# Performance work log

Measured on AMD Instinct MI355X. Metric: run time of the kernel, lower is better.

Reference implementation:

```python
import jax, jax.numpy as jnp
import numpy as np

B, D, L, H = 2, 64, 512, 1024  # batch, n_docs (timesteps), tokens per doc, bert hidden


def _ln(x, g, b):
    # torch.nn.LayerNorm over last dim, eps=1e-5
    m = jnp.mean(x, axis=-1, keepdims=True)
    v = jnp.mean((x - m) ** 2, axis=-1, keepdims=True)
    return (x - m) / jnp.sqrt(v + 1e-5) * g + b


def _ht(x):
    # Hardtanh(min=-8, max=8)
    return jnp.clip(x, -8.0, 8.0)


def setup_inputs() -> dict:
    key = jax.random.key(0)
    ks = jax.random.split(key, 12)
    xavier = lambda k, shape: jax.random.normal(k, shape, dtype=jnp.float32) * np.float32(np.sqrt(2.0 / sum(shape)))
    return {
        "trans": jax.random.normal(ks[0], (B, D, L, H), dtype=jnp.float32) * 0.1,  # frozen BERT last_hidden_state
        "document_mask": jax.random.bernoulli(ks[1], 0.9, (B, D)),
        "Wf": xavier(ks[2], (H, H)), "bf": jnp.ones((H,), jnp.float32),
        "Wi": xavier(ks[3], (H, H)), "bi": jnp.zeros((H,), jnp.float32),
        "Wg": xavier(ks[4], (H, H)), "bg": jnp.zeros((H,), jnp.float32),
        "Wo": xavier(ks[5], (H, H)), "bo": jnp.zeros((H,), jnp.float32),
        "Wp": xavier(ks[6], (H, H)), "bp": jnp.zeros((H,), jnp.float32),
        "tF": xavier(ks[7], (L,)), "tI": xavier(ks[8], (L,)), "tO": xavier(ks[9], (L,)),
        "c_gamma": jnp.ones((H,), jnp.float32), "c_beta": jnp.zeros((H,), jnp.float32),
        "h_gamma": jnp.ones((H,), jnp.float32), "h_beta": jnp.zeros((H,), jnp.float32),
    }


def _forward(trans, document_mask, Wf, bf, Wi, bi, Wg, bg, Wo, bo, Wp, bp,
             tF, tI, tO, c_gamma, c_beta, h_gamma, h_beta):
    b, d, l, h = trans.shape
    # docFlat @ transform: contract the token (l) axis -> [b, d, h]
    pF = jnp.einsum('bdlh,l->bdh', trans, tF)
    pI = jnp.einsum('bdlh,l->bdh', trans, tI)
    pO = jnp.einsum('bdlh,l->bdh', trans, tO)

    def step(carry, xs):
        c, hs = carry                      # each [b, h]
        pf, pi, po, m = xs                 # [b, h] x3, [b] bool
        nC = _ln(c, c_gamma, c_beta)
        nH = _ln(hs, h_gamma, h_beta)
        f = jax.nn.sigmoid(_ht(nH @ Wf.T + bf) + pf)
        c2 = c * f
        i = jax.nn.sigmoid(_ht(nH @ Wi.T + bi) + pi)
        g = _ht(jax.nn.gelu(nH @ Wg.T + bg, approximate=False) + pi)
        c2 = c2 + i * g
        o = jax.nn.sigmoid(_ht(nH @ Wo.T + bo) + po)
        h2 = o * _ht(jax.nn.gelu(nC @ Wp.T + bp, approximate=False))
        mm = m[:, None]
        h2 = jnp.where(mm, h2, hs)
        c2 = jnp.where(mm, c2, c)
        c2 = jnp.clip(c2, -10.0, 10.0)
        h2 = jnp.clip(h2, -10.0, 10.0)
        return (c2, h2), None

    init = (jnp.zeros((b, h), trans.dtype), jnp.zeros((b, h), trans.dtype))
    xs = (pF.transpose(1, 0, 2), pI.transpose(1, 0, 2), pO.transpose(1, 0, 2), document_mask.T)
    (c_fin, h_fin), _ = jax.lax.scan(step, init, xs)
    return h_fin  # [b, h] (original returns [b, h, 1])


def reference(trans, document_mask, Wf, bf, Wi, bi, Wg, bg, Wo, bo, Wp, bp,
              tF, tI, tO, c_gamma, c_beta, h_gamma, h_beta):
    return _forward(trans, document_mask, Wf, bf, Wi, bi, Wg, bg, Wo, bo, Wp, bp,
                    tF, tI, tO, c_gamma, c_beta, h_gamma, h_beta)
```

## Files before the change

### kernel.cpp

```cpp
#include <hip/hip_runtime.h>
#include <math.h>


#define NBLK 256
typedef unsigned long long u64;

__device__ __forceinline__ float sigf(float x)   { return 1.0f / (1.0f + __expf(-x)); }
__device__ __forceinline__ float geluf(float x)  { return 0.5f * x * (1.0f + erff(x * 0.70710678118654752f)); }
__device__ __forceinline__ float clampf(float x, float lo, float hi) { return fminf(fmaxf(x, lo), hi); }

__device__ __forceinline__ void astf(float* p, float v) {
    __hip_atomic_store(p, v, __ATOMIC_RELAXED, __HIP_MEMORY_SCOPE_AGENT);
}
__device__ __forceinline__ float aldf(const float* p) {
    return __hip_atomic_load(p, __ATOMIC_RELAXED, __HIP_MEMORY_SCOPE_AGENT);
}
__device__ __forceinline__ void astu(unsigned* p, unsigned v) {
    __hip_atomic_store(p, v, __ATOMIC_RELAXED, __HIP_MEMORY_SCOPE_AGENT);
}
__device__ __forceinline__ unsigned aldu(const unsigned* p) {
    return __hip_atomic_load(p, __ATOMIC_RELAXED, __HIP_MEMORY_SCOPE_AGENT);
}
__device__ __forceinline__ void ast64(u64* p, u64 v) {
    __hip_atomic_store(p, v, __ATOMIC_RELAXED, __HIP_MEMORY_SCOPE_AGENT);
}
__device__ __forceinline__ u64 ald64(const u64* p) {
    return __hip_atomic_load(p, __ATOMIC_RELAXED, __HIP_MEMORY_SCOPE_AGENT);
}

__device__ __forceinline__ void gridbar(unsigned tgt, unsigned* flags, unsigned* rel,
                                        int blk, int t) {
    __syncthreads();
    if (t == 0) astu(&flags[blk], tgt);
    if (blk == 0) {
        if (t < 64) {
            for (;;) {
                unsigned a = aldu(&flags[t]);
                unsigned b = aldu(&flags[t + 64]);
                unsigned c = aldu(&flags[t + 128]);
                unsigned d = aldu(&flags[t + 192]);
                int ok = (a >= tgt) && (b >= tgt) && (c >= tgt) && (d >= tgt);
                if (__all(ok)) break;
                __builtin_amdgcn_s_sleep(1);
            }
            if (t == 0) astu(rel, tgt);
        }
    } else if (t == 0) {
        while (aldu(rel) < tgt) __builtin_amdgcn_s_sleep(2);
    }
    __syncthreads();
}

__global__ __launch_bounds__(256, 1) void fused_kernel(
    const float* __restrict__ trans, const int* __restrict__ mask,
    const float* __restrict__ Wf, const float* __restrict__ bf,
    const float* __restrict__ Wi, const float* __restrict__ bi,
    const float* __restrict__ Wg, const float* __restrict__ bg,
    const float* __restrict__ Wo, const float* __restrict__ bo,
    const float* __restrict__ Wp, const float* __restrict__ bp,
    const float* __restrict__ tF, const float* __restrict__ tI, const float* __restrict__ tO,
    const float* __restrict__ c_gamma, const float* __restrict__ c_beta,
    const float* __restrict__ h_gamma, const float* __restrict__ h_beta,
    float* __restrict__ ws, float* __restrict__ out)
{
    const int t    = threadIdx.x;
    const int lane = t & 63;
    const int wv   = t >> 6;
    const int blk  = blockIdx.x;
    const int hrow = (blk << 2) + wv;

    unsigned* flags = (unsigned*)ws;
    unsigned* rel   = flags + 256;
    u64* stC2 = (u64*)(ws + 320);
    u64* stH2 = (u64*)(ws + 8512);
    float* pF  = ws + 16704;
    float* pI  = pF + 131072;
    float* pO  = pI + 131072;

    __shared__ float smem[2][4][1024];
    __shared__ float red[2][4][8];

    float4 wfr[4], wir[4], wgr[4], wor[4], wpr[4];
    {
        const float4* rf = (const float4*)(Wf + (size_t)hrow * 1024);
        const float4* ri = (const float4*)(Wi + (size_t)hrow * 1024);
        const float4* rg = (const float4*)(Wg + (size_t)hrow * 1024);
        const float4* ro = (const float4*)(Wo + (size_t)hrow * 1024);
        const float4* rp = (const float4*)(Wp + (size_t)hrow * 1024);
        #pragma unroll
        for (int q = 0; q < 4; ++q) {
            const int k4 = lane + 64 * q;
            wfr[q] = rf[k4]; wir[q] = ri[k4]; wgr[q] = rg[k4];
            wor[q] = ro[k4]; wpr[q] = rp[k4];
        }
    }
    const float bfv = bf[hrow], biv = bi[hrow], bgv = bg[hrow], bov = bo[hrow], bpv = bp[hrow];

    {
        float* sF = &smem[0][0][0];
        float* sI = &smem[0][0][512];
        float* sO = &smem[0][1][0];
        sF[t] = tF[t]; sF[t + 256] = tF[t + 256];
        sI[t] = tI[t]; sI[t + 256] = tI[t + 256];
        sO[t] = tO[t]; sO[t + 256] = tO[t + 256];
        __syncthreads();

        const int bd = blk >> 1;
        const int h0 = (blk & 1) * 512;
        const int s  = t & 127;
        const int g  = t >> 7;
        const float4* tr = (const float4*)trans + (size_t)bd * 512 * 256 + (h0 >> 2) + s;

        float4 aF = make_float4(0.f,0.f,0.f,0.f);
        float4 aI = make_float4(0.f,0.f,0.f,0.f);
        float4 aO = make_float4(0.f,0.f,0.f,0.f);
        #pragma unroll 8
        for (int li = 0; li < 256; ++li) {
            const int l = g + 2 * li;
            float4 v = tr[(size_t)l * 256];
            const float wf = sF[l], wi = sI[l], wo = sO[l];
            aF.x = fmaf(v.x, wf, aF.x); aF.y = fmaf(v.y, wf, aF.y);
            aF.z = fmaf(v.z, wf, aF.z); aF.w = fmaf(v.w, wf, aF.w);
            aI.x = fmaf(v.x, wi, aI.x); aI.y = fmaf(v.y, wi, aI.y);
            aI.z = fmaf(v.z, wi, aI.z); aI.w = fmaf(v.w, wi, aI.w);
            aO.x = fmaf(v.x, wo, aO.x); aO.y = fmaf(v.y, wo, aO.y);
            aO.z = fmaf(v.z, wo, aO.z); aO.w = fmaf(v.w, wo, aO.w);
        }
        float4* cmb = (float4*)&smem[0][2][0];
        if (g == 1) { cmb[s] = aF; cmb[128 + s] = aI; cmb[256 + s] = aO; }
        __syncthreads();
        if (g == 0) {
            const float4 bF = cmb[s], bI = cmb[128 + s], bO = cmb[256 + s];
            aF.x += bF.x; aF.y += bF.y; aF.z += bF.z; aF.w += bF.w;
            aI.x += bI.x; aI.y += bI.y; aI.z += bI.z; aI.w += bI.w;
            aO.x += bO.x; aO.y += bO.y; aO.z += bO.z; aO.w += bO.w;
            const int base = bd * 1024 + h0 + 4 * s;
            astf(&pF[base+0], aF.x); astf(&pF[base+1], aF.y);
            astf(&pF[base+2], aF.z); astf(&pF[base+3], aF.w);
            astf(&pI[base+0], aI.x); astf(&pI[base+1], aI.y);
            astf(&pI[base+2], aI.z); astf(&pI[base+3], aI.w);
            astf(&pO[base+0], aO.x); astf(&pO[base+1], aO.y);
            astf(&pO[base+2], aO.z); astf(&pO[base+3], aO.w);
        }
    }
    gridbar(1u, flags, rel, blk, t);

    float cgv[4], cbv[4], hgv[4], hbv[4];
    #pragma unroll
    for (int j = 0; j < 4; ++j) {
        const int e = t + 256 * j;
        cgv[j] = c_gamma[e]; cbv[j] = c_beta[e];
        hgv[j] = h_gamma[e]; hbv[j] = h_beta[e];
    }

    for (int d = 0; d < 64; ++d) {
        const int par = d & 1;
        const u64* cc2 = stC2 + par * 2048;
        const u64* hc2 = stH2 + par * 2048;
        u64* cn2 = stC2 + (par ^ 1) * 2048;
        u64* hn2 = stH2 + (par ^ 1) * 2048;
        float (*sm)[1024] = smem[par];
        float (*rd)[8]    = red[par];

        float pfv = 0.f, piv = 0.f, pov = 0.f;
        if (lane < 2) {
            const int pidx = (lane * 64 + d) * 1024 + hrow;
            pfv = aldf(&pF[pidx]); piv = aldf(&pI[pidx]); pov = aldf(&pO[pidx]);
        }

        u64 vc0[4], vc1[4], vh0[4], vh1[4];
        u64 vco = 0, vho = 0;
        const unsigned dtag = (unsigned)d;
        for (;;) {
            #pragma unroll
            for (int j = 0; j < 4; ++j) {
                const int e = t + 256 * j;
                vc0[j] = ald64(cc2 + e);        vc1[j] = ald64(cc2 + 1024 + e);
                vh0[j] = ald64(hc2 + e);        vh1[j] = ald64(hc2 + 1024 + e);
            }
            bool ok = true;
            #pragma unroll
            for (int j = 0; j < 4; ++j) {
                ok = ok && ((unsigned)(vc0[j] >> 32) == dtag) && ((unsigned)(vc1[j] >> 32) == dtag)
                        && ((unsigned)(vh0[j] >> 32) == dtag) && ((unsigned)(vh1[j] >> 32) == dtag);
            }
            if (lane < 2) {
                vco = ald64(cc2 + lane * 1024 + hrow);
                vho = ald64(hc2 + lane * 1024 + hrow);
                ok = ok && ((unsigned)(vco >> 32) == dtag) && ((unsigned)(vho >> 32) == dtag);
            }
            if (ok) break;
            __builtin_amdgcn_s_sleep(1);
        }

        float cv0[4], cv1[4], hv0[4], hv1[4];
        float s0=0,s1=0,s2=0,s3=0,s4=0,s5=0,s6=0,s7=0;
        #pragma unroll
        for (int j = 0; j < 4; ++j) {
            cv0[j] = __uint_as_float((unsigned)vc0[j]);
            cv1[j] = __uint_as_float((unsigned)vc1[j]);
            hv0[j] = __uint_as_float((unsigned)vh0[j]);
            hv1[j] = __uint_as_float((unsigned)vh1[j]);
            s0 += cv0[j]; s1 += cv0[j]*cv0[j];
            s2 += cv1[j]; s3 += cv1[j]*cv1[j];
            s4 += hv0[j]; s5 += hv0[j]*hv0[j];
            s6 += hv1[j]; s7 += hv1[j]*hv1[j];
        }
        #pragma unroll
        for (int off = 32; off; off >>= 1) {
            s0 += __shfl_xor(s0, off); s1 += __shfl_xor(s1, off);
            s2 += __shfl_xor(s2, off); s3 += __shfl_xor(s3, off);
            s4 += __shfl_xor(s4, off); s5 += __shfl_xor(s5, off);
            s6 += __shfl_xor(s6, off); s7 += __shfl_xor(s7, off);
        }
        if (lane == 0) {
            rd[wv][0]=s0; rd[wv][1]=s1; rd[wv][2]=s2; rd[wv][3]=s3;
            rd[wv][4]=s4; rd[wv][5]=s5; rd[wv][6]=s6; rd[wv][7]=s7;
        }
        __syncthreads();
        const float tc0 = rd[0][0]+rd[1][0]+rd[2][0]+rd[3][0];
        const float qc0 = rd[0][1]+rd[1][1]+rd[2][1]+rd[3][1];
        const float tc1 = rd[0][2]+rd[1][2]+rd[2][2]+rd[3][2];
        const float qc1 = rd[0][3]+rd[1][3]+rd[2][3]+rd[3][3];
        const float th0 = rd[0][4]+rd[1][4]+rd[2][4]+rd[3][4];
        const float qh0 = rd[0][5]+rd[1][5]+rd[2][5]+rd[3][5];
        const float th1 = rd[0][6]+rd[1][6]+rd[2][6]+rd[3][6];
        const float qh1 = rd[0][7]+rd[1][7]+rd[2][7]+rd[3][7];
        const float inv = 1.0f / 1024.0f;
        const float mc0 = tc0*inv, rc0 = rsqrtf(qc0*inv - mc0*mc0 + 1e-5f);
        const float mc1 = tc1*inv, rc1 = rsqrtf(qc1*inv - mc1*mc1 + 1e-5f);
        const float mh0 = th0*inv, rh0 = rsqrtf(qh0*inv - mh0*mh0 + 1e-5f);
        const float mh1 = th1*inv, rh1 = rsqrtf(qh1*inv - mh1*mh1 + 1e-5f);

        #pragma unroll
        for (int j = 0; j < 4; ++j) {
            const int e = t + 256 * j;
            sm[0][e] = (hv0[j]-mh0)*rh0*hgv[j] + hbv[j];
            sm[1][e] = (hv1[j]-mh1)*rh1*hgv[j] + hbv[j];
            sm[2][e] = (cv0[j]-mc0)*rc0*cgv[j] + cbv[j];
            sm[3][e] = (cv1[j]-mc1)*rc1*cgv[j] + cbv[j];
        }
        __syncthreads();

        float zf0=0,zf1=0,zi0=0,zi1=0,zg0=0,zg1=0,zo0=0,zo1=0,zp0=0,zp1=0;
        #pragma unroll
        for (int q = 0; q < 4; ++q) {
            const int k4 = lane + 64 * q;
            const float4 n0 = ((const float4*)sm[0])[k4];
            const float4 n1 = ((const float4*)sm[1])[k4];
            const float4 m0 = ((const float4*)sm[2])[k4];
            const float4 m1 = ((const float4*)sm[3])[k4];
            zf0 += wfr[q].x*n0.x + wfr[q].y*n0.y + wfr[q].z*n0.z + wfr[q].w*n0.w;
            zf1 += wfr[q].x*n1.x + wfr[q].y*n1.y + wfr[q].z*n1.z + wfr[q].w*n1.w;
            zi0 += wir[q].x*n0.x + wir[q].y*n0.y + wir[q].z*n0.z + wir[q].w*n0.w;
            zi1 += wir[q].x*n1.x + wir[q].y*n1.y + wir[q].z*n1.z + wir[q].w*n1.w;
            zg0 += wgr[q].x*n0.x + wgr[q].y*n0.y + wgr[q].z*n0.z + wgr[q].w*n0.w;
            zg1 += wgr[q].x*n1.x + wgr[q].y*n1.y + wgr[q].z*n1.z + wgr[q].w*n1.w;
            zo0 += wor[q].x*n0.x + wor[q].y*n0.y + wor[q].z*n0.z + wor[q].w*n0.w;
            zo1 += wor[q].x*n1.x + wor[q].y*n1.y + wor[q].z*n1.z + wor[q].w*n1.w;
            zp0 += wpr[q].x*m0.x + wpr[q].y*m0.y + wpr[q].z*m0.z + wpr[q].w*m0.w;
            zp1 += wpr[q].x*m1.x + wpr[q].y*m1.y + wpr[q].z*m1.z + wpr[q].w*m1.w;
        }
        #pragma unroll
        for (int off = 32; off; off >>= 1) {
            zf0 += __shfl_xor(zf0, off); zf1 += __shfl_xor(zf1, off);
            zi0 += __shfl_xor(zi0, off); zi1 += __shfl_xor(zi1, off);
            zg0 += __shfl_xor(zg0, off); zg1 += __shfl_xor(zg1, off);
            zo0 += __shfl_xor(zo0, off); zo1 += __shfl_xor(zo1, off);
            zp0 += __shfl_xor(zp0, off); zp1 += __shfl_xor(zp1, off);
        }

        if (lane < 2) {
            const int b = lane;
            const float zf = b ? zf1 : zf0;
            const float zi = b ? zi1 : zi0;
            const float zg = b ? zg1 : zg0;
            const float zo = b ? zo1 : zo0;
            const float zp = b ? zp1 : zp0;
            const float f  = sigf(clampf(zf + bfv, -8.f, 8.f) + pfv);
            const float ig = sigf(clampf(zi + biv, -8.f, 8.f) + piv);
            const float g  = clampf(geluf(zg + bgv) + piv, -8.f, 8.f);
            const float o  = sigf(clampf(zo + bov, -8.f, 8.f) + pov);
            const float hp = clampf(geluf(zp + bpv), -8.f, 8.f);
            const float co = __uint_as_float((unsigned)vco);
            const float ho = __uint_as_float((unsigned)vho);
            float c2 = co * f + ig * g;
            float h2 = o * hp;
            if (mask[b * 64 + d] == 0) { c2 = co; h2 = ho; }
            c2 = clampf(c2, -10.f, 10.f);
            h2 = clampf(h2, -10.f, 10.f);
            if (d == 63) {
                out[b * 1024 + hrow] = h2;
            } else {
                const u64 tg = ((u64)(unsigned)(d + 1)) << 32;
                ast64(cn2 + b * 1024 + hrow, tg | (u64)__float_as_uint(c2));
                ast64(hn2 + b * 1024 + hrow, tg | (u64)__float_as_uint(h2));
            }
        }
    }
}

extern "C" void kernel_launch(void* const* d_in, const int* in_sizes, int n_in,
                              void* d_out, int out_size, void* d_ws, size_t ws_size,
                              hipStream_t stream)
{
    const float* trans = (const float*)d_in[0];
    const int*   mask  = (const int*)d_in[1];
    const float* Wf = (const float*)d_in[2];  const float* bf = (const float*)d_in[3];
    const float* Wi = (const float*)d_in[4];  const float* bi = (const float*)d_in[5];
    const float* Wg = (const float*)d_in[6];  const float* bg = (const float*)d_in[7];
    const float* Wo = (const float*)d_in[8];  const float* bo = (const float*)d_in[9];
    const float* Wp = (const float*)d_in[10]; const float* bp = (const float*)d_in[11];
    const float* tF = (const float*)d_in[12];
    const float* tI = (const float*)d_in[13];
    const float* tO = (const float*)d_in[14];
    const float* c_gamma = (const float*)d_in[15];
    const float* c_beta  = (const float*)d_in[16];
    const float* h_gamma = (const float*)d_in[17];
    const float* h_beta  = (const float*)d_in[18];

    float* ws  = (float*)d_ws;
    float* out = (float*)d_out;

    hipMemsetAsync(d_ws, 0, 16704u * sizeof(float), stream);

    void* args[] = { (void*)&trans, (void*)&mask,
                     (void*)&Wf, (void*)&bf, (void*)&Wi, (void*)&bi,
                     (void*)&Wg, (void*)&bg, (void*)&Wo, (void*)&bo,
                     (void*)&Wp, (void*)&bp,
                     (void*)&tF, (void*)&tI, (void*)&tO,
                     (void*)&c_gamma, (void*)&c_beta, (void*)&h_gamma, (void*)&h_beta,
                     (void*)&ws, (void*)&out };
    hipLaunchCooperativeKernel((void*)fused_kernel, dim3(256), dim3(256), args, 0, stream);
}
```

Before: 966.5 us.

## Replace tagged 64-bit state polling with per-block flag barrier and fold LayerNorm into weights

Each step now waits on a per-block flag array polled by one wave, instead of every thread spinning on tag-packed 64-bit state loads. Plain 32-bit state values are read after the flag check. LayerNorm gamma/beta are folded into the register-resident weight rows once, and mean/rstd are applied to the dot-product results as a scalar correction. This drops a shared-memory pass and a __syncthreads per step. Per-step synchronization now needs a full flag wait plus extra block barriers, and the algebraic LayerNorm fold can change rounding slightly.

```diff
diff --git a/kernel.cpp b/kernel.cpp
--- a/kernel.cpp
+++ b/kernel.cpp
@@ -3,7 +3,6 @@
 
 
 #define NBLK 256
-typedef unsigned long long u64;
 
 __device__ __forceinline__ float sigf(float x)   { return 1.0f / (1.0f + __expf(-x)); }
 __device__ __forceinline__ float geluf(float x)  { return 0.5f * x * (1.0f + erff(x * 0.70710678118654752f)); }
@@ -20,35 +19,6 @@
 }
 __device__ __forceinline__ unsigned aldu(const unsigned* p) {
     return __hip_atomic_load(p, __ATOMIC_RELAXED, __HIP_MEMORY_SCOPE_AGENT);
-}
-__device__ __forceinline__ void ast64(u64* p, u64 v) {
-    __hip_atomic_store(p, v, __ATOMIC_RELAXED, __HIP_MEMORY_SCOPE_AGENT);
-}
-__device__ __forceinline__ u64 ald64(const u64* p) {
-    return __hip_atomic_load(p, __ATOMIC_RELAXED, __HIP_MEMORY_SCOPE_AGENT);
-}
-
-__device__ __forceinline__ void gridbar(unsigned tgt, unsigned* flags, unsigned* rel,
-                                        int blk, int t) {
-    __syncthreads();
-    if (t == 0) astu(&flags[blk], tgt);
-    if (blk == 0) {
-        if (t < 64) {
-            for (;;) {
-                unsigned a = aldu(&flags[t]);
-                unsigned b = aldu(&flags[t + 64]);
-                unsigned c = aldu(&flags[t + 128]);
-                unsigned d = aldu(&flags[t + 192]);
-                int ok = (a >= tgt) && (b >= tgt) && (c >= tgt) && (d >= tgt);
-                if (__all(ok)) break;
-                __builtin_amdgcn_s_sleep(1);
-            }
-            if (t == 0) astu(rel, tgt);
-        }
-    } else if (t == 0) {
-        while (aldu(rel) < tgt) __builtin_amdgcn_s_sleep(2);
-    }
-    __syncthreads();
 }
 
 __global__ __launch_bounds__(256, 1) void fused_kernel(
@@ -70,10 +40,9 @@
     const int hrow = (blk << 2) + wv;
 
     unsigned* flags = (unsigned*)ws;
-    unsigned* rel   = flags + 256;
-    u64* stC2 = (u64*)(ws + 320);
-    u64* stH2 = (u64*)(ws + 8512);
-    float* pF  = ws + 16704;
+    float* stC = ws + 320;
+    float* stH = ws + 4416;
+    float* pF  = ws + 8512;
     float* pI  = pF + 131072;
     float* pO  = pI + 131072;
 
@@ -143,64 +112,117 @@
             astf(&pO[base+2], aO.z); astf(&pO[base+3], aO.w);
         }
     }
-    gridbar(1u, flags, rel, blk, t);
-
-    float cgv[4], cbv[4], hgv[4], hbv[4];
-    #pragma unroll
-    for (int j = 0; j < 4; ++j) {
-        const int e = t + 256 * j;
-        cgv[j] = c_gamma[e]; cbv[j] = c_beta[e];
-        hgv[j] = h_gamma[e]; hbv[j] = h_beta[e];
-    }
+    __syncthreads();
+    if (t == 0) astu(&flags[blk], 1u);
+
+    float sfv, siv, sgv, sov, spv, bfb, bib, bgb, bob, bpb;
+    {
+        float4 gh4[4], bh4[4], gc4[4], bc4[4];
+        const float4* Gh = (const float4*)h_gamma;
+        const float4* Bh = (const float4*)h_beta;
+        const float4* Gc = (const float4*)c_gamma;
+        const float4* Bc = (const float4*)c_beta;
+        #pragma unroll
+        for (int q = 0; q < 4; ++q) {
+            const int k4 = lane + 64 * q;
+            gh4[q] = Gh[k4]; bh4[q] = Bh[k4]; gc4[q] = Gc[k4]; bc4[q] = Bc[k4];
+        }
+        bfb = bib = bgb = bob = bpb = 0.f;
+        #pragma unroll
+        for (int q = 0; q < 4; ++q) {
+            bfb += wfr[q].x*bh4[q].x + wfr[q].y*bh4[q].y + wfr[q].z*bh4[q].z + wfr[q].w*bh4[q].w;
+            bib += wir[q].x*bh4[q].x + wir[q].y*bh4[q].y + wir[q].z*bh4[q].z + wir[q].w*bh4[q].w;
+            bgb += wgr[q].x*bh4[q].x + wgr[q].y*bh4[q].y + wgr[q].z*bh4[q].z + wgr[q].w*bh4[q].w;
+            bob += wor[q].x*bh4[q].x + wor[q].y*bh4[q].y + wor[q].z*bh4[q].z + wor[q].w*bh4[q].w;
+            bpb += wpr[q].x*bc4[q].x + wpr[q].y*bc4[q].y + wpr[q].z*bc4[q].z + wpr[q].w*bc4[q].w;
+        }
+        #pragma unroll
+        for (int q = 0; q < 4; ++q) {
+            wfr[q].x *= gh4[q].x; wfr[q].y *= gh4[q].y; wfr[q].z *= gh4[q].z; wfr[q].w *= gh4[q].w;
+            wir[q].x *= gh4[q].x; wir[q].y *= gh4[q].y; wir[q].z *= gh4[q].z; wir[q].w *= gh4[q].w;
+            wgr[q].x *= gh4[q].x; wgr[q].y *= gh4[q].y; wgr[q].z *= gh4[q].z; wgr[q].w *= gh4[q].w;
+            wor[q].x *= gh4[q].x; wor[q].y *= gh4[q].y; wor[q].z *= gh4[q].z; wor[q].w *= gh4[q].w;
+            wpr[q].x *= gc4[q].x; wpr[q].y *= gc4[q].y; wpr[q].z *= gc4[q].z; wpr[q].w *= gc4[q].w;
+        }
+        sfv = siv = sgv = sov = spv = 0.f;
+        #pragma unroll
+        for (int q = 0; q < 4; ++q) {
+            sfv += wfr[q].x + wfr[q].y + wfr[q].z + wfr[q].w;
+            siv += wir[q].x + wir[q].y + wir[q].z + wir[q].w;
+            sgv += wgr[q].x + wgr[q].y + wgr[q].z + wgr[q].w;
+            sov += wor[q].x + wor[q].y + wor[q].z + wor[q].w;
+            spv += wpr[q].x + wpr[q].y + wpr[q].z + wpr[q].w;
+        }
+        #pragma unroll
+        for (int off = 32; off; off >>= 1) {
+            sfv += __shfl_xor(sfv, off); siv += __shfl_xor(siv, off);
+            sgv += __shfl_xor(sgv, off); sov += __shfl_xor(sov, off);
+            spv += __shfl_xor(spv, off);
+            bfb += __shfl_xor(bfb, off); bib += __shfl_xor(bib, off);
+            bgb += __shfl_xor(bgb, off); bob += __shfl_xor(bob, off);
+            bpb += __shfl_xor(bpb, off);
+        }
+    }
+
+    if (wv == 0) {
+        for (;;) {
+            const unsigned a0 = aldu(&flags[lane]);
+            const unsigned a1 = aldu(&flags[lane + 64]);
+            const unsigned a2 = aldu(&flags[lane + 128]);
+            const unsigned a3 = aldu(&flags[lane + 192]);
+            const int ok = (a0 >= 1u) && (a1 >= 1u) && (a2 >= 1u) && (a3 >= 1u);
+            if (__all(ok)) break;
+            __builtin_amdgcn_s_sleep(1);
+        }
+    }
+    __syncthreads();
+
+    float c_prev = 0.f, h_prev = 0.f;
 
     for (int d = 0; d < 64; ++d) {
         const int par = d & 1;
-        const u64* cc2 = stC2 + par * 2048;
-        const u64* hc2 = stH2 + par * 2048;
-        u64* cn2 = stC2 + (par ^ 1) * 2048;
-        u64* hn2 = stH2 + (par ^ 1) * 2048;
+        const float* cc = stC + par * 2048;
+        const float* hc = stH + par * 2048;
+        float* cn = stC + (par ^ 1) * 2048;
+        float* hn = stH + (par ^ 1) * 2048;
         float (*sm)[1024] = smem[par];
         float (*rd)[8]    = red[par];
 
         float pfv = 0.f, piv = 0.f, pov = 0.f;
+        int mv = 1;
         if (lane < 2) {
             const int pidx = (lane * 64 + d) * 1024 + hrow;
             pfv = aldf(&pF[pidx]); piv = aldf(&pI[pidx]); pov = aldf(&pO[pidx]);
-        }
-
-        u64 vc0[4], vc1[4], vh0[4], vh1[4];
-        u64 vco = 0, vho = 0;
-        const unsigned dtag = (unsigned)d;
-        for (;;) {
-            #pragma unroll
-            for (int j = 0; j < 4; ++j) {
-                const int e = t + 256 * j;
-                vc0[j] = ald64(cc2 + e);        vc1[j] = ald64(cc2 + 1024 + e);
-                vh0[j] = ald64(hc2 + e);        vh1[j] = ald64(hc2 + 1024 + e);
+            mv = mask[lane * 64 + d];
+        }
+
+        if (wv == 0) {
+            const unsigned tgt = (unsigned)(d + 1);
+            for (;;) {
+                const unsigned a0 = aldu(&flags[lane]);
+                const unsigned a1 = aldu(&flags[lane + 64]);
+                const unsigned a2 = aldu(&flags[lane + 128]);
+                const unsigned a3 = aldu(&flags[lane + 192]);
+                const int ok = (a0 >= tgt) && (a1 >= tgt) && (a2 >= tgt) && (a3 >= tgt);
+                if (__all(ok)) break;
+                __builtin_amdgcn_s_sleep(1);
             }
-            bool ok = true;
-            #pragma unroll
-            for (int j = 0; j < 4; ++j) {
-                ok = ok && ((unsigned)(vc0[j] >> 32) == dtag) && ((unsigned)(vc1[j] >> 32) == dtag)
-                        && ((unsigned)(vh0[j] >> 32) == dtag) && ((unsigned)(vh1[j] >> 32) == dtag);
-            }
-            if (lane < 2) {
-                vco = ald64(cc2 + lane * 1024 + hrow);
-                vho = ald64(hc2 + lane * 1024 + hrow);
-                ok = ok && ((unsigned)(vco >> 32) == dtag) && ((unsigned)(vho >> 32) == dtag);
-            }
-            if (ok) break;
-            __builtin_amdgcn_s_sleep(1);
-        }
+        }
+        __syncthreads();
 
         float cv0[4], cv1[4], hv0[4], hv1[4];
+        #pragma unroll
+        for (int j = 0; j < 4; ++j) {
+            const int e = t + 256 * j;
+            cv0[j] = aldf(cc + e);        cv1[j] = aldf(cc + 1024 + e);
+            hv0[j] = aldf(hc + e);        hv1[j] = aldf(hc + 1024 + e);
+        }
         float s0=0,s1=0,s2=0,s3=0,s4=0,s5=0,s6=0,s7=0;
         #pragma unroll
         for (int j = 0; j < 4; ++j) {
-            cv0[j] = __uint_as_float((unsigned)vc0[j]);
-            cv1[j] = __uint_as_float((unsigned)vc1[j]);
-            hv0[j] = __uint_as_float((unsigned)vh0[j]);
-            hv1[j] = __uint_as_float((unsigned)vh1[j]);
+            const int e = t + 256 * j;
+            sm[0][e] = hv0[j]; sm[1][e] = hv1[j];
+            sm[2][e] = cv0[j]; sm[3][e] = cv1[j];
             s0 += cv0[j]; s1 += cv0[j]*cv0[j];
             s2 += cv1[j]; s3 += cv1[j]*cv1[j];
             s4 += hv0[j]; s5 += hv0[j]*hv0[j];
@@ -218,6 +240,7 @@
             rd[wv][4]=s4; rd[wv][5]=s5; rd[wv][6]=s6; rd[wv][7]=s7;
         }
         __syncthreads();
+
         const float tc0 = rd[0][0]+rd[1][0]+rd[2][0]+rd[3][0];
         const float qc0 = rd[0][1]+rd[1][1]+rd[2][1]+rd[3][1];
         const float tc1 = rd[0][2]+rd[1][2]+rd[2][2]+rd[3][2];
@@ -231,16 +254,6 @@
         const float mc1 = tc1*inv, rc1 = rsqrtf(qc1*inv - mc1*mc1 + 1e-5f);
         const float mh0 = th0*inv, rh0 = rsqrtf(qh0*inv - mh0*mh0 + 1e-5f);
         const float mh1 = th1*inv, rh1 = rsqrtf(qh1*inv - mh1*mh1 + 1e-5f);
-
-        #pragma unroll
-        for (int j = 0; j < 4; ++j) {
-            const int e = t + 256 * j;
-            sm[0][e] = (hv0[j]-mh0)*rh0*hgv[j] + hbv[j];
-            sm[1][e] = (hv1[j]-mh1)*rh1*hgv[j] + hbv[j];
-            sm[2][e] = (cv0[j]-mc0)*rc0*cgv[j] + cbv[j];
-            sm[3][e] = (cv1[j]-mc1)*rc1*cgv[j] + cbv[j];
-        }
-        __syncthreads();
 
         float zf0=0,zf1=0,zi0=0,zi1=0,zg0=0,zg1=0,zo0=0,zo1=0,zp0=0,zp1=0;
         #pragma unroll
@@ -272,31 +285,35 @@
 
         if (lane < 2) {
             const int b = lane;
-            const float zf = b ? zf1 : zf0;
-            const float zi = b ? zi1 : zi0;
-            const float zg = b ? zg1 : zg0;
-            const float zo = b ? zo1 : zo0;
-            const float zp = b ? zp1 : zp0;
+            const float mh = b ? mh1 : mh0, rh = b ? rh1 : rh0;
+            const float mc = b ? mc1 : mc0, rc = b ? rc1 : rc0;
+            const float zf = rh * ((b ? zf1 : zf0) - mh * sfv) + bfb;
+            const float zi = rh * ((b ? zi1 : zi0) - mh * siv) + bib;
+            const float zg = rh * ((b ? zg1 : zg0) - mh * sgv) + bgb;
+            const float zo = rh * ((b ? zo1 : zo0) - mh * sov) + bob;
+            const float zp = rc * ((b ? zp1 : zp0) - mc * spv) + bpb;
             const float f  = sigf(clampf(zf + bfv, -8.f, 8.f) + pfv);
             const float ig = sigf(clampf(zi + biv, -8.f, 8.f) + piv);
             const float g  = clampf(geluf(zg + bgv) + piv, -8.f, 8.f);
             const float o  = sigf(clampf(zo + bov, -8.f, 8.f) + pov);
             const float hp = clampf(geluf(zp + bpv), -8.f, 8.f);
-            const float co = __uint_as_float((unsigned)vco);
-            const float ho = __uint_as_float((unsigned)vho);
-            float c2 = co * f + ig * g;
+            float c2 = c_prev * f + ig * g;
             float h2 = o * hp;
-            if (mask[b * 64 + d] == 0) { c2 = co; h2 = ho; }
+            if (mv == 0) { c2 = c_prev; h2 = h_prev; }
             c2 = clampf(c2, -10.f, 10.f);
             h2 = clampf(h2, -10.f, 10.f);
+            c_prev = c2; h_prev = h2;
             if (d == 63) {
                 out[b * 1024 + hrow] = h2;
             } else {
-                const u64 tg = ((u64)(unsigned)(d + 1)) << 32;
-                ast64(cn2 + b * 1024 + hrow, tg | (u64)__float_as_uint(c2));
-                ast64(hn2 + b * 1024 + hrow, tg | (u64)__float_as_uint(h2));
+                astf(cn + b * 1024 + hrow, c2);
+                astf(hn + b * 1024 + hrow, h2);
             }
         }
+
+        if (d == 63) break;
+        __syncthreads();
+        if (t == 0) astu(&flags[blk], (unsigned)(d + 2));
     }
 }
 
@@ -322,7 +339,7 @@
     float* ws  = (float*)d_ws;
     float* out = (float*)d_out;
 
-    hipMemsetAsync(d_ws, 0, 16704u * sizeof(float), stream);
+    hipMemsetAsync(d_ws, 0, 8512u * sizeof(float), stream);
 
     void* args[] = { (void*)&trans, (void*)&mask,
                      (void*)&Wf, (void*)&bf, (void*)&Wi, (void*)&bi,
```

Result: faster. 895.7 us (-7.3%).
